# Optimization experiments

Hardware: AMD Instinct MI355X
Metric: run time of the kernel (lower is better)

## Reference

```python
import jax, jax.numpy as jnp
import numpy as np

DIM = 1024
CTX_DIM = 1024
HEADS = 16
DIM_HEAD = 64
INNER = HEADS * DIM_HEAD  # 1024
FF_INNER = 4 * DIM        # 4096
EPS = 1e-5


def layer_norm(x, g, b):
    mu = jnp.mean(x, axis=-1, keepdims=True)
    var = jnp.var(x, axis=-1, keepdims=True)
    return (x - mu) * jax.lax.rsqrt(var + EPS) * g + b


def setup_inputs() -> dict:
    key = jax.random.key(0)
    ks = jax.random.split(key, 9)
    b, n, j = 4, 2048, 1024
    inp = {
        "x": jax.random.normal(ks[0], (b, n, DIM), dtype=jnp.float32),
        "context": jax.random.normal(ks[1], (b, j, CTX_DIM), dtype=jnp.float32),
        "ln_g": jnp.ones((DIM,), jnp.float32),
        "ln_b": jnp.zeros((DIM,), jnp.float32),
        "cln_g": jnp.ones((CTX_DIM,), jnp.float32),
        "cln_b": jnp.zeros((CTX_DIM,), jnp.float32),
        "Wq": jax.random.normal(ks[2], (DIM, INNER), dtype=jnp.float32) * (DIM ** -0.5),
        "Wkv": jax.random.normal(ks[3], (CTX_DIM, 2 * DIM_HEAD), dtype=jnp.float32) * (CTX_DIM ** -0.5),
        "Wo": jax.random.normal(ks[4], (INNER, DIM), dtype=jnp.float32) * (INNER ** -0.5),
        "Wff1": jax.random.normal(ks[5], (DIM, 2 * FF_INNER), dtype=jnp.float32) * (DIM ** -0.5),
        "Wff2": jax.random.normal(ks[6], (FF_INNER, DIM), dtype=jnp.float32) * (FF_INNER ** -0.5),
    }
    return inp


def reference(x, context, ln_g, ln_b, cln_g, cln_b, Wq, Wkv, Wo, Wff1, Wff2):
    scale = DIM_HEAD ** -0.5
    xn = layer_norm(x, ln_g, ln_b)                       # [b, n, dim]
    cn = layer_norm(context, cln_g, cln_b)               # [b, j, ctx_dim]
    b, n, _ = xn.shape
    q = (xn @ Wq).reshape(b, n, HEADS, DIM_HEAD).transpose(0, 2, 1, 3) * scale  # [b,h,n,d]
    kv = cn @ Wkv                                        # [b, j, 2d]
    k, v = kv[..., :DIM_HEAD], kv[..., DIM_HEAD:]        # [b, j, d] each (shared head)
    sim = jnp.einsum('bhid,bjd->bhij', q, k)
    attn = jax.nn.softmax(sim, axis=-1)
    out = jnp.einsum('bhij,bjd->bhid', attn, v)          # [b,h,n,d]
    out = out.transpose(0, 2, 1, 3).reshape(b, n, INNER) @ Wo  # [b,n,dim]
    # parallel SwiGLU FF on normed x
    ff = xn @ Wff1                                       # [b,n,2*ff_inner]
    h, gate = ff[..., :FF_INNER], ff[..., FF_INNER:]
    out = out + (jax.nn.silu(gate) * h) @ Wff2
    return out
```

## Files before the change

kernel.cpp:

```cpp
#include <hip/hip_runtime.h>
#include <math.h>

typedef unsigned short u16;
typedef __attribute__((ext_vector_type(8))) short short8;
typedef __attribute__((ext_vector_type(8))) unsigned short ushortx8;
typedef __attribute__((ext_vector_type(4))) unsigned short ushortx4;
typedef __attribute__((ext_vector_type(4))) float floatx4;

#define DEVI __device__ __forceinline__

DEVI float bf2f(u16 u) {
    unsigned int i = ((unsigned int)u) << 16;
    float f; __builtin_memcpy(&f, &i, 4); return f;
}
DEVI u16 f2bf(float f) {
    unsigned int i; __builtin_memcpy(&i, &f, 4);
    i += 0x7fffu + ((i >> 16) & 1u);
    return (u16)(i >> 16);
}
DEVI void gl_lds16(const void* g, void* l) {
    __builtin_amdgcn_global_load_lds(
        (const __attribute__((address_space(1))) void*)g,
        (__attribute__((address_space(3))) void*)l, 16, 0, 0);
}

__global__ void transpose_kernel(const float* __restrict__ B, u16* __restrict__ BT,
                                 int K, int N) {
    __shared__ u16 t[32][33];
    int nb = blockIdx.x * 32, kb = blockIdx.y * 32;
    int tx = threadIdx.x, ty = threadIdx.y;
    for (int i = ty; i < 32; i += 8)
        t[i][tx] = f2bf(B[(size_t)(kb + i) * N + nb + tx]);
    __syncthreads();
    for (int i = ty; i < 32; i += 8)
        BT[(size_t)(nb + i) * K + kb + tx] = t[tx][i];
}

__global__ __launch_bounds__(256)
void ln_kernel(const float* __restrict__ x, const float* __restrict__ g,
               const float* __restrict__ b, u16* __restrict__ out) {
    __shared__ float sw[4], sw2[4];
    const int tid = threadIdx.x, wave = tid >> 6, lane = tid & 63;
    const float* xr = x + (size_t)blockIdx.x * 1024;
    float4 v = *(const float4*)(xr + tid * 4);
    float f[4] = {v.x, v.y, v.z, v.w};
    float s = f[0] + f[1] + f[2] + f[3];
    float s2 = f[0]*f[0] + f[1]*f[1] + f[2]*f[2] + f[3]*f[3];
    for (int o = 32; o; o >>= 1) {
        s  += __shfl_xor(s,  o, 64);
        s2 += __shfl_xor(s2, o, 64);
    }
    if (lane == 0) { sw[wave] = s; sw2[wave] = s2; }
    __syncthreads();
    float tot  = sw[0] + sw[1] + sw[2] + sw[3];
    float tot2 = sw2[0] + sw2[1] + sw2[2] + sw2[3];
    float mu  = tot * (1.f / 1024.f);
    float var = tot2 * (1.f / 1024.f) - mu * mu;
    float rs  = rsqrtf(var + 1e-5f);
    float4 gv = *(const float4*)(g + tid * 4);
    float4 bv = *(const float4*)(b + tid * 4);
    ushortx4 ov;
    ov[0] = f2bf((f[0] - mu) * rs * gv.x + bv.x);
    ov[1] = f2bf((f[1] - mu) * rs * gv.y + bv.y);
    ov[2] = f2bf((f[2] - mu) * rs * gv.z + bv.z);
    ov[3] = f2bf((f[3] - mu) * rs * gv.w + bv.w);
    *(ushortx4*)(out + (size_t)blockIdx.x * 1024 + tid * 4) = ov;
}

enum { EPI_PLAIN = 0, EPI_Q = 1, EPI_KV = 2, EPI_ADD_F32 = 3 };

template <int EPI>
__global__ __launch_bounds__(256)
void gemm_bt_kernel(const u16* __restrict__ A, const u16* __restrict__ BT,
                    void* __restrict__ Cv, u16* __restrict__ AUX,
                    int M, int N, int K) {
    __shared__ u16 As[128 * 32];
    __shared__ u16 Bs[128 * 32];
    const int tid = threadIdx.x, wave = tid >> 6, lane = tid & 63;
    const int mbase = blockIdx.x * 128, nbase = blockIdx.y * 128;
    const int m0 = (wave & 1) * 64, n0 = (wave >> 1) * 64;
    const int lrow = lane & 15, lq = lane >> 4;

    floatx4 zero = {0.f, 0.f, 0.f, 0.f};
    floatx4 acc[4][4];
#pragma unroll
    for (int i = 0; i < 4; i++)
#pragma unroll
        for (int j = 0; j < 4; j++) acc[i][j] = zero;

    for (int kt = 0; kt < K; kt += 32) {
#pragma unroll
        for (int i = 0; i < 2; i++) {
            int e = i * 2048 + tid * 8;
            int r = e >> 5, c = e & 31;
            gl_lds16(A  + (size_t)(mbase + r) * K + kt + c, As + e);
            gl_lds16(BT + (size_t)(nbase + r) * K + kt + c, Bs + e);
        }
        __syncthreads();
        short8 af[4], bf[4];
#pragma unroll
        for (int f = 0; f < 4; f++) {
            af[f] = *(const short8*)(As + (m0 + f * 16 + lrow) * 32 + lq * 8);
            bf[f] = *(const short8*)(Bs + (n0 + f * 16 + lrow) * 32 + lq * 8);
        }
#pragma unroll
        for (int i = 0; i < 4; i++)
#pragma unroll
            for (int j = 0; j < 4; j++)
                acc[i][j] = __builtin_amdgcn_mfma_f32_16x16x32_bf16(af[i], bf[j], acc[i][j], 0, 0, 0);
        __syncthreads();
    }

#pragma unroll
    for (int mf = 0; mf < 4; mf++)
#pragma unroll
        for (int nf = 0; nf < 4; nf++)
#pragma unroll
            for (int r = 0; r < 4; r++) {
                int row = mbase + m0 + mf * 16 + lq * 4 + r;
                int col = nbase + n0 + nf * 16 + lrow;
                float v = acc[mf][nf][r];
                if constexpr (EPI == EPI_PLAIN) {
                    ((u16*)Cv)[(size_t)row * N + col] = f2bf(v);
                } else if constexpr (EPI == EPI_Q) {
                    int b = row >> 11, i2 = row & 2047, h = col >> 6, d = col & 63;
                    ((u16*)Cv)[((size_t)((b * 16 + h) * 2048 + i2)) * 64 + d] = f2bf(v * 0.125f);
                } else if constexpr (EPI == EPI_KV) {
                    int b = row >> 10, j = row & 1023;
                    if (col < 64) ((u16*)Cv)[(size_t)row * 64 + col] = f2bf(v);
                    else AUX[((size_t)(b * 64 + (col - 64))) * 1024 + j] = f2bf(v);
                } else {
                    ((float*)Cv)[(size_t)row * N + col] = v + bf2f(AUX[(size_t)row * N + col]);
                }
            }
}

__global__ __launch_bounds__(512)
void gemm_ff1_kernel(const u16* __restrict__ A, const u16* __restrict__ BTh,
                     const u16* __restrict__ BTg, u16* __restrict__ Cact,
                     int K, int Nout) {
    __shared__ u16 As[256 * 32];
    __shared__ u16 Bh[64 * 32];
    __shared__ u16 Bg[64 * 32];
    const int tid = threadIdx.x, wave = tid >> 6, lane = tid & 63;
    const int mbase = blockIdx.x * 256, nbase = blockIdx.y * 64;
    const int m0 = (wave & 3) * 64, n0 = (wave >> 2) * 32;
    const int lrow = lane & 15, lq = lane >> 4;

    floatx4 zero = {0.f, 0.f, 0.f, 0.f};
    floatx4 ah[4][2], ag[4][2];
#pragma unroll
    for (int i = 0; i < 4; i++)
#pragma unroll
        for (int j = 0; j < 2; j++) { ah[i][j] = zero; ag[i][j] = zero; }

    for (int kt = 0; kt < K; kt += 32) {
#pragma unroll
        for (int i = 0; i < 2; i++) {
            int e = i * 4096 + tid * 8;
            int r = e >> 5, c = e & 31;
            gl_lds16(A + (size_t)(mbase + r) * K + kt + c, As + e);
        }
        {
            int e = (tid & 255) * 8;
            int r = e >> 5, c = e & 31;
            const u16* src = (tid < 256) ? BTh : BTg;
            u16* dst = (tid < 256) ? Bh : Bg;
            gl_lds16(src + (size_t)(nbase + r) * K + kt + c, dst + e);
        }
        __syncthreads();
        short8 af[4], bhf[2], bgf[2];
#pragma unroll
        for (int f = 0; f < 4; f++)
            af[f] = *(const short8*)(As + (m0 + f * 16 + lrow) * 32 + lq * 8);
#pragma unroll
        for (int f = 0; f < 2; f++) {
            bhf[f] = *(const short8*)(Bh + (n0 + f * 16 + lrow) * 32 + lq * 8);
            bgf[f] = *(const short8*)(Bg + (n0 + f * 16 + lrow) * 32 + lq * 8);
        }
#pragma unroll
        for (int i = 0; i < 4; i++)
#pragma unroll
            for (int j = 0; j < 2; j++) {
                ah[i][j] = __builtin_amdgcn_mfma_f32_16x16x32_bf16(af[i], bhf[j], ah[i][j], 0, 0, 0);
                ag[i][j] = __builtin_amdgcn_mfma_f32_16x16x32_bf16(af[i], bgf[j], ag[i][j], 0, 0, 0);
            }
        __syncthreads();
    }

#pragma unroll
    for (int mf = 0; mf < 4; mf++)
#pragma unroll
        for (int nf = 0; nf < 2; nf++)
#pragma unroll
            for (int r = 0; r < 4; r++) {
                int row = mbase + m0 + mf * 16 + lq * 4 + r;
                int col = nbase + n0 + nf * 16 + lrow;
                float hv = ah[mf][nf][r], gv = ag[mf][nf][r];
                float act = hv * (gv / (1.f + __expf(-gv)));
                Cact[(size_t)row * Nout + col] = f2bf(act);
            }
}

__global__ __launch_bounds__(256)
void attn_kernel(const u16* __restrict__ q, const u16* __restrict__ k,
                 const u16* __restrict__ vt, u16* __restrict__ o) {
    __shared__ char smem[53248];
    u16* Qs  = (u16*)smem;
    u16* Ps  = (u16*)smem;
    u16* Ks  = (u16*)(smem + 17408);
    u16* VTs = (u16*)(smem + 35840);
    float* Lp   = (float*)(smem + 17408);
    float* Ltot = (float*)(smem + 18432);

    const int tid = threadIdx.x, wave = tid >> 6, lane = tid & 63;
    const int lrow = lane & 15, lq = lane >> 4;
    const int b = blockIdx.z, h = blockIdx.y, mt = blockIdx.x;

    const u16* qb = q + ((size_t)((b * 16 + h) * 2048) + mt * 64) * 64;
    const u16* kb = k + (size_t)b * 1024 * 64;
    const u16* vb = vt + (size_t)b * 64 * 1024;

#pragma unroll
    for (int i = 0; i < 2; i++) {
        int e = i * 2048 + tid * 8;
        int r = e >> 6, d = e & 63;
        *(ushortx8*)(Qs + r * 72 + d) = *(const ushortx8*)(qb + e);
    }
    __syncthreads();
    short8 qf[2][4];
#pragma unroll
    for (int ks = 0; ks < 2; ks++)
#pragma unroll
        for (int cf = 0; cf < 4; cf++)
            qf[ks][cf] = *(const short8*)(Qs + (cf * 16 + lrow) * 72 + ks * 32 + lq * 8);

    floatx4 zero = {0.f, 0.f, 0.f, 0.f};
    floatx4 oacc[4];
#pragma unroll
    for (int i = 0; i < 4; i++) oacc[i] = zero;
    float lsum[4] = {0.f, 0.f, 0.f, 0.f};

    for (int jt = 0; jt < 8; jt++) {
#pragma unroll
        for (int i = 0; i < 4; i++) {
            int e = i * 2048 + tid * 8;
            int r = e >> 6, d = e & 63;
            *(ushortx8*)(Ks + r * 72 + d) = *(const ushortx8*)(kb + jt * 8192 + e);
            int dv = e >> 7, jj = e & 127;
            *(ushortx8*)(VTs + dv * 136 + jj) =
                *(const ushortx8*)(vb + (size_t)dv * 1024 + jt * 128 + jj);
        }
        __syncthreads();

        floatx4 sacc[2][4];
#pragma unroll
        for (int rf = 0; rf < 2; rf++)
#pragma unroll
            for (int cf = 0; cf < 4; cf++) sacc[rf][cf] = zero;
#pragma unroll
        for (int ks = 0; ks < 2; ks++) {
            short8 af[2];
#pragma unroll
            for (int rf = 0; rf < 2; rf++)
                af[rf] = *(const short8*)(Ks + (wave * 32 + rf * 16 + lrow) * 72 + ks * 32 + lq * 8);
#pragma unroll
            for (int rf = 0; rf < 2; rf++)
#pragma unroll
                for (int cf = 0; cf < 4; cf++)
                    sacc[rf][cf] = __builtin_amdgcn_mfma_f32_16x16x32_bf16(af[rf], qf[ks][cf], sacc[rf][cf], 0, 0, 0);
        }

#pragma unroll
        for (int rf = 0; rf < 2; rf++)
#pragma unroll
            for (int cf = 0; cf < 4; cf++) {
                float p0 = __expf(sacc[rf][cf][0]);
                float p1 = __expf(sacc[rf][cf][1]);
                float p2 = __expf(sacc[rf][cf][2]);
                float p3 = __expf(sacc[rf][cf][3]);
                lsum[cf] += p0 + p1 + p2 + p3;
                ushortx4 pk = {f2bf(p0), f2bf(p1), f2bf(p2), f2bf(p3)};
                int m = cf * 16 + lrow;
                int j0 = wave * 32 + rf * 16 + lq * 4;
                *(ushortx4*)(Ps + m * 136 + j0) = pk;
            }
        __syncthreads();

#pragma unroll
        for (int ks = 0; ks < 4; ks++) {
            short8 pf[4];
#pragma unroll
            for (int mf = 0; mf < 4; mf++)
                pf[mf] = *(const short8*)(Ps + (mf * 16 + lrow) * 136 + ks * 32 + lq * 8);
            short8 vf = *(const short8*)(VTs + (wave * 16 + lrow) * 136 + ks * 32 + lq * 8);
#pragma unroll
            for (int mf = 0; mf < 4; mf++)
                oacc[mf] = __builtin_amdgcn_mfma_f32_16x16x32_bf16(pf[mf], vf, oacc[mf], 0, 0, 0);
        }
        __syncthreads();
    }

    float lv[4];
#pragma unroll
    for (int cf = 0; cf < 4; cf++) {
        float v = lsum[cf];
        v += __shfl_xor(v, 16, 64);
        v += __shfl_xor(v, 32, 64);
        lv[cf] = v;
    }
    if (lane < 16) {
#pragma unroll
        for (int cf = 0; cf < 4; cf++) Lp[wave * 64 + cf * 16 + lane] = lv[cf];
    }
    __syncthreads();
    if (tid < 64) Ltot[tid] = Lp[tid] + Lp[64 + tid] + Lp[128 + tid] + Lp[192 + tid];
    __syncthreads();

    const int d = wave * 16 + lrow;
    const size_t orow0 = (size_t)(b * 2048 + mt * 64);
#pragma unroll
    for (int mf = 0; mf < 4; mf++)
#pragma unroll
        for (int r = 0; r < 4; r++) {
            int m = mf * 16 + lq * 4 + r;
            float val = oacc[mf][r] / Ltot[m];
            o[(orow0 + m) * 1024 + h * 64 + d] = f2bf(val);
        }
}

extern "C" void kernel_launch(void* const* d_in, const int* in_sizes, int n_in,
                              void* d_out, int out_size, void* d_ws, size_t ws_size,
                              hipStream_t stream) {
    const float* x     = (const float*)d_in[0];
    const float* ctx   = (const float*)d_in[1];
    const float* ln_g  = (const float*)d_in[2];
    const float* ln_b  = (const float*)d_in[3];
    const float* cln_g = (const float*)d_in[4];
    const float* cln_b = (const float*)d_in[5];
    const float* Wq    = (const float*)d_in[6];
    const float* Wkv   = (const float*)d_in[7];
    const float* Wo    = (const float*)d_in[8];
    const float* Wff1  = (const float*)d_in[9];
    const float* Wff2  = (const float*)d_in[10];
    (void)in_sizes; (void)n_in; (void)out_size; (void)ws_size;

    u16* ws = (u16*)d_ws;
    const size_t MiB = 524288;
    u16* ffa   = ws;
    u16* qb    = ws;
    u16* attnb = ws + 16 * MiB;
    u16* cn    = ws + 32 * MiB;
    u16* kb    = ws + 40 * MiB;
    u16* vtb   = ws + 40 * MiB + 262144;
    u16* WqT   = ws + 41 * MiB;
    u16* WkvT  = ws + 43 * MiB;
    u16* WoT   = ws + 44 * MiB;
    u16* xn    = ws + 64 * MiB;
    u16* wo    = ws + 80 * MiB;
    u16* Wff1T = ws + 96 * MiB;
    u16* Wff2T = ws + 112 * MiB;

    dim3 tb(32, 8);
    transpose_kernel<<<dim3(32, 32),  tb, 0, stream>>>(Wq,   WqT,   1024, 1024);
    transpose_kernel<<<dim3(4, 32),   tb, 0, stream>>>(Wkv,  WkvT,  1024, 128);
    transpose_kernel<<<dim3(32, 32),  tb, 0, stream>>>(Wo,   WoT,   1024, 1024);
    transpose_kernel<<<dim3(256, 32), tb, 0, stream>>>(Wff1, Wff1T, 1024, 8192);
    transpose_kernel<<<dim3(32, 128), tb, 0, stream>>>(Wff2, Wff2T, 4096, 1024);

    ln_kernel<<<8192, 256, 0, stream>>>(x,   ln_g,  ln_b,  xn);
    ln_kernel<<<4096, 256, 0, stream>>>(ctx, cln_g, cln_b, cn);

    gemm_bt_kernel<EPI_Q> <<<dim3(64, 8), 256, 0, stream>>>(xn, WqT,  qb, nullptr, 8192, 1024, 1024);
    gemm_bt_kernel<EPI_KV><<<dim3(32, 1), 256, 0, stream>>>(cn, WkvT, kb, vtb,     4096, 128,  1024);

    attn_kernel<<<dim3(32, 16, 4), 256, 0, stream>>>(qb, kb, vtb, attnb);

    gemm_bt_kernel<EPI_PLAIN><<<dim3(64, 8), 256, 0, stream>>>(attnb, WoT, wo, nullptr, 8192, 1024, 1024);
    gemm_ff1_kernel<<<dim3(32, 64), 512, 0, stream>>>(xn, Wff1T, Wff1T + (size_t)4096 * 1024, ffa, 1024, 4096);
    gemm_bt_kernel<EPI_ADD_F32><<<dim3(64, 8), 256, 0, stream>>>(ffa, Wff2T, d_out, wo, 8192, 1024, 4096);
}
```

Before: 597.1 us.

## Rewrite FF1 GEMM with 256x256 tiles, interleaved h/gate weights, pipelined LDS

The Wff1 transpose now interleaves the h and gate weight rows in 16-row groups, so one B tile holds both halves. The FF1 SwiGLU GEMM becomes a 256x256-tile kernel with a 4-deep LDS ring (two stages prefetched), XOR-swizzled LDS layout, grouped block ordering for L2 reuse, and setprio around the MFMAs. The goal is to raise arithmetic intensity per tile and hide global-load latency that the previous single-buffered 256x64 kernel exposed. In exchange it needs 128 KiB of dynamic LDS, a larger register footprint, and hand-written waitcnt-based synchronisation.

```diff
diff --git a/kernel.cpp b/kernel.cpp
--- a/kernel.cpp
+++ b/kernel.cpp
@@ -24,6 +24,7 @@
         (__attribute__((address_space(3))) void*)l, 16, 0, 0);
 }
 
+template <bool FF1>
 __global__ void transpose_kernel(const float* __restrict__ B, u16* __restrict__ BT,
                                  int K, int N) {
     __shared__ u16 t[32][33];
@@ -32,8 +33,11 @@
     for (int i = ty; i < 32; i += 8)
         t[i][tx] = f2bf(B[(size_t)(kb + i) * N + nb + tx]);
     __syncthreads();
-    for (int i = ty; i < 32; i += 8)
-        BT[(size_t)(nb + i) * K + kb + tx] = t[tx][i];
+    for (int i = ty; i < 32; i += 8) {
+        int c = nb + i;
+        int r_out = FF1 ? ((((c & 4095) >> 4) << 5) + ((c >> 12) << 4) + (c & 15)) : c;
+        BT[(size_t)r_out * K + kb + tx] = t[tx][i];
+    }
 }
 
 __global__ __launch_bounds__(256)
@@ -135,70 +139,91 @@
             }
 }
 
-__global__ __launch_bounds__(512)
-void gemm_ff1_kernel(const u16* __restrict__ A, const u16* __restrict__ BTh,
-                     const u16* __restrict__ BTg, u16* __restrict__ Cact,
-                     int K, int Nout) {
-    __shared__ u16 As[256 * 32];
-    __shared__ u16 Bh[64 * 32];
-    __shared__ u16 Bg[64 * 32];
+__global__ __launch_bounds__(512, 2)
+void gemm256_ff1_kernel(const u16* __restrict__ A, const u16* __restrict__ BT,
+                        u16* __restrict__ C, int K) {
+    extern __shared__ float4 smem4[];
+    char* smem = (char*)smem4;
+
     const int tid = threadIdx.x, wave = tid >> 6, lane = tid & 63;
-    const int mbase = blockIdx.x * 256, nbase = blockIdx.y * 64;
-    const int m0 = (wave & 3) * 64, n0 = (wave >> 2) * 32;
+    const int wm = wave >> 2, wn = wave & 3;
     const int lrow = lane & 15, lq = lane >> 4;
 
+    const int bid = blockIdx.x;
+    const int wg = (bid & 7) * 128 + (bid >> 3);
+    const int mbase = (wg & 31) * 256, nbase = (wg >> 5) * 256;
+
+    const int srow  = tid >> 2;
+    const int sslot = (tid & 3) ^ ((tid >> 3) & 3);
+    const u16* aS = A  + (size_t)(mbase + srow) * K + sslot * 8;
+    const u16* bS = BT + (size_t)(nbase + srow) * K + sslot * 8;
+    const size_t chunkK = (size_t)128 * K;
+    char* dst0 = smem + tid * 16;
+
+#define STAGE(t_, kt_) do {                                   \
+        char* db_ = dst0 + ((t_) & 3) * 32768;                \
+        gl_lds16(aS + (kt_),          db_);                   \
+        gl_lds16(aS + chunkK + (kt_), db_ + 8192);            \
+        gl_lds16(bS + (kt_),          db_ + 16384);           \
+        gl_lds16(bS + chunkK + (kt_), db_ + 24576);           \
+    } while (0)
+
     floatx4 zero = {0.f, 0.f, 0.f, 0.f};
-    floatx4 ah[4][2], ag[4][2];
-#pragma unroll
-    for (int i = 0; i < 4; i++)
-#pragma unroll
-        for (int j = 0; j < 2; j++) { ah[i][j] = zero; ag[i][j] = zero; }
-
-    for (int kt = 0; kt < K; kt += 32) {
-#pragma unroll
-        for (int i = 0; i < 2; i++) {
-            int e = i * 4096 + tid * 8;
-            int r = e >> 5, c = e & 31;
-            gl_lds16(A + (size_t)(mbase + r) * K + kt + c, As + e);
-        }
-        {
-            int e = (tid & 255) * 8;
-            int r = e >> 5, c = e & 31;
-            const u16* src = (tid < 256) ? BTh : BTg;
-            u16* dst = (tid < 256) ? Bh : Bg;
-            gl_lds16(src + (size_t)(nbase + r) * K + kt + c, dst + e);
-        }
-        __syncthreads();
-        short8 af[4], bhf[2], bgf[2];
-#pragma unroll
-        for (int f = 0; f < 4; f++)
-            af[f] = *(const short8*)(As + (m0 + f * 16 + lrow) * 32 + lq * 8);
-#pragma unroll
-        for (int f = 0; f < 2; f++) {
-            bhf[f] = *(const short8*)(Bh + (n0 + f * 16 + lrow) * 32 + lq * 8);
-            bgf[f] = *(const short8*)(Bg + (n0 + f * 16 + lrow) * 32 + lq * 8);
-        }
-#pragma unroll
-        for (int i = 0; i < 4; i++)
-#pragma unroll
-            for (int j = 0; j < 2; j++) {
-                ah[i][j] = __builtin_amdgcn_mfma_f32_16x16x32_bf16(af[i], bhf[j], ah[i][j], 0, 0, 0);
-                ag[i][j] = __builtin_amdgcn_mfma_f32_16x16x32_bf16(af[i], bgf[j], ag[i][j], 0, 0, 0);
-            }
-        __syncthreads();
-    }
-
-#pragma unroll
-    for (int mf = 0; mf < 4; mf++)
-#pragma unroll
-        for (int nf = 0; nf < 2; nf++)
-#pragma unroll
-            for (int r = 0; r < 4; r++) {
-                int row = mbase + m0 + mf * 16 + lq * 4 + r;
-                int col = nbase + n0 + nf * 16 + lrow;
-                float hv = ah[mf][nf][r], gv = ag[mf][nf][r];
+    floatx4 acc[8][4];
+#pragma unroll
+    for (int i = 0; i < 8; i++)
+#pragma unroll
+        for (int j = 0; j < 4; j++) acc[i][j] = zero;
+
+    const int NT = K >> 5;
+    STAGE(0, 0);
+    STAGE(1, 32);
+
+    const int swb = (lq ^ ((lrow >> 1) & 3)) * 16;
+    const int aRow = wm * 128 + lrow;
+    const int bRow = wn * 64 + lrow;
+
+    for (int t = 0; t < NT; ++t) {
+        if (t + 1 < NT) { asm volatile("s_waitcnt vmcnt(4)" ::: "memory"); }
+        else            { asm volatile("s_waitcnt vmcnt(0)" ::: "memory"); }
+        asm volatile("s_waitcnt lgkmcnt(0)" ::: "memory");
+        __builtin_amdgcn_s_barrier();
+        asm volatile("" ::: "memory");
+
+        if (t + 2 < NT) STAGE(t + 2, (t + 2) * 32);
+
+        const char* buf = smem + (t & 3) * 32768;
+        const char* Ab = buf + (size_t)aRow * 64 + swb;
+        const char* Bb = buf + 16384 + (size_t)bRow * 64 + swb;
+        short8 af[8], bf[4];
+#pragma unroll
+        for (int mf = 0; mf < 8; ++mf) af[mf] = *(const short8*)(Ab + mf * 1024);
+#pragma unroll
+        for (int nf = 0; nf < 4; ++nf) bf[nf] = *(const short8*)(Bb + nf * 1024);
+
+        __builtin_amdgcn_s_setprio(1);
+#pragma unroll
+        for (int mf = 0; mf < 8; ++mf)
+#pragma unroll
+            for (int nf = 0; nf < 4; ++nf)
+                acc[mf][nf] = __builtin_amdgcn_mfma_f32_16x16x32_bf16(af[mf], bf[nf], acc[mf][nf], 0, 0, 0);
+        __builtin_amdgcn_s_setprio(0);
+    }
+#undef STAGE
+
+    const int orow0 = mbase + wm * 128;
+    const int pcol0 = (nbase + wn * 64) >> 1;
+#pragma unroll
+    for (int mf = 0; mf < 8; ++mf)
+#pragma unroll
+        for (int p = 0; p < 2; ++p)
+#pragma unroll
+            for (int r = 0; r < 4; ++r) {
+                float hv = acc[mf][2 * p][r], gv = acc[mf][2 * p + 1][r];
                 float act = hv * (gv / (1.f + __expf(-gv)));
-                Cact[(size_t)row * Nout + col] = f2bf(act);
+                int row = orow0 + mf * 16 + lq * 4 + r;
+                int col = pcol0 + p * 16 + lrow;
+                C[(size_t)row * 4096 + col] = f2bf(act);
             }
 }
 
@@ -361,12 +386,19 @@
     u16* Wff1T = ws + 96 * MiB;
     u16* Wff2T = ws + 112 * MiB;
 
+    static bool attr_set = false;
+    if (!attr_set) {
+        hipFuncSetAttribute(reinterpret_cast<const void*>(gemm256_ff1_kernel),
+                            hipFuncAttributeMaxDynamicSharedMemorySize, 131072);
+        attr_set = true;
+    }
+
     dim3 tb(32, 8);
-    transpose_kernel<<<dim3(32, 32),  tb, 0, stream>>>(Wq,   WqT,   1024, 1024);
-    transpose_kernel<<<dim3(4, 32),   tb, 0, stream>>>(Wkv,  WkvT,  1024, 128);
-    transpose_kernel<<<dim3(32, 32),  tb, 0, stream>>>(Wo,   WoT,   1024, 1024);
-    transpose_kernel<<<dim3(256, 32), tb, 0, stream>>>(Wff1, Wff1T, 1024, 8192);
-    transpose_kernel<<<dim3(32, 128), tb, 0, stream>>>(Wff2, Wff2T, 4096, 1024);
+    transpose_kernel<false><<<dim3(32, 32),  tb, 0, stream>>>(Wq,   WqT,   1024, 1024);
+    transpose_kernel<false><<<dim3(4, 32),   tb, 0, stream>>>(Wkv,  WkvT,  1024, 128);
+    transpose_kernel<false><<<dim3(32, 32),  tb, 0, stream>>>(Wo,   WoT,   1024, 1024);
+    transpose_kernel<true> <<<dim3(256, 32), tb, 0, stream>>>(Wff1, Wff1T, 1024, 8192);
+    transpose_kernel<false><<<dim3(32, 128), tb, 0, stream>>>(Wff2, Wff2T, 4096, 1024);
 
     ln_kernel<<<8192, 256, 0, stream>>>(x,   ln_g,  ln_b,  xn);
     ln_kernel<<<4096, 256, 0, stream>>>(ctx, cln_g, cln_b, cn);
@@ -377,6 +409,6 @@
     attn_kernel<<<dim3(32, 16, 4), 256, 0, stream>>>(qb, kb, vtb, attnb);
 
     gemm_bt_kernel<EPI_PLAIN><<<dim3(64, 8), 256, 0, stream>>>(attnb, WoT, wo, nullptr, 8192, 1024, 1024);
-    gemm_ff1_kernel<<<dim3(32, 64), 512, 0, stream>>>(xn, Wff1T, Wff1T + (size_t)4096 * 1024, ffa, 1024, 4096);
+    gemm256_ff1_kernel<<<dim3(1024), 512, 131072, stream>>>(xn, Wff1T, ffa, 1024);
     gemm_bt_kernel<EPI_ADD_F32><<<dim3(64, 8), 256, 0, stream>>>(ffa, Wff2T, d_out, wo, 8192, 1024, 4096);
 }
```

Measured after the change: 590.2 us. Within noise of the previous version (-1.2%).
